# Optimization experiments

Measured on AMD Instinct MI355X. Metric: run time of the kernel, lower is better.

## Reference

```python
import jax, jax.numpy as jnp
import numpy as np

B, L, H, NE, SPAN = 16, 2048, 768, 64, 4
EPS_COS = 1e-8   # torch cosine_similarity eps
EPS_STD = 1e-5   # std stabilizer from the module


def _linear_init(key, fan_in, fan_out):
    s = 1.0 / np.sqrt(fan_in)
    kw, kb = jax.random.split(key)
    w = jax.random.uniform(kw, (fan_in, fan_out), jnp.float32, -s, s)
    b = jax.random.uniform(kb, (fan_out,), jnp.float32, -s, s)
    return w, b


def setup_inputs() -> dict:
    key = jax.random.key(0)
    ks = jax.random.split(key, 6)
    w1, b1 = _linear_init(ks[0], 2 * H + 1, H)
    w2, b2 = _linear_init(ks[1], H, 512)
    w3, b3 = _linear_init(ks[2], 512, 256)
    w4, b4 = _linear_init(ks[3], 256, 2)
    x = jax.random.normal(ks[4], (B, L, H), jnp.float32)
    entity_starts = jax.random.randint(ks[5], (B, NE), 0, L - SPAN)
    threshold = jnp.float32(0.9)
    return dict(x=x, threshold=threshold,
                w1=w1, b1=b1, w2=w2, b2=b2, w3=w3, b3=b3, w4=w4, b4=b4,
                entity_starts=entity_starts)


def reference(x, threshold, w1, b1, w2, b2, w3, b3, w4, b4, entity_starts):
    # --- per-entity span max-pool (segment-max over x) ---
    # gather span tokens: [B, NE*SPAN] token indices into the L axis
    idx = (entity_starts[:, :, None] + jnp.arange(SPAN)).reshape(B, NE * SPAN)
    spans = jnp.take_along_axis(x, idx[:, :, None], axis=1)      # [B, NE*SPAN, H]
    emb = spans.reshape(B, NE, SPAN, H).max(axis=2)               # [B, NE, H]

    # --- pairwise cosine similarity per batch ---
    norm = jnp.maximum(jnp.linalg.norm(emb, axis=-1, keepdims=True), EPS_COS)
    n = emb / norm
    cos = jnp.einsum('bie,bje->bij', n, n)                        # [B, NE, NE]
    std = jnp.std(cos, axis=(1, 2), ddof=1, keepdims=True)        # torch .std() is unbiased
    sim = (cos - threshold) / (std + EPS_STD)
    sim = jnp.triu(sim, k=1)

    # --- all i<j pairs: [sim, emb_i, emb_j] ---
    iu, ju = np.triu_indices(NE, k=1)                             # static pair indices
    feats = jnp.concatenate(
        [sim[:, iu, ju, None], emb[:, iu, :], emb[:, ju, :]], axis=-1
    ).reshape(-1, 2 * H + 1)                                      # [B*P, 2H+1]

    # --- classifier MLP (dropout = identity at eval) ---
    h = jax.nn.relu(feats @ w1 + b1)
    h = jax.nn.relu(h @ w2 + b2)
    h = jax.nn.relu(h @ w3 + b3)
    logits = h @ w4 + b4                                          # [B*P, 2]
    return logits
```

## Files before the change

### kernel.cpp

```cpp
#include <hip/hip_runtime.h>
#include <cstdint>
#include <cstddef>

#define B_    16
#define L_    2048
#define H_    768
#define NE_   64
#define SPAN_ 4
#define NPAIR 2016
#define NROWS (B_ * NPAIR)

typedef __bf16 bf16_t;
typedef __bf16 bf16x8 __attribute__((ext_vector_type(8)));
typedef __bf16 bf16x4 __attribute__((ext_vector_type(4)));
typedef float  floatx4 __attribute__((ext_vector_type(4)));

#define OFF_EMBH   ((size_t)3145728)
#define OFF_SIM    ((size_t)8126464)
#define OFF_W1ABT  ((size_t)8255488)
#define OFF_W2T    ((size_t)10614784)
#define OFF_W3T    ((size_t)11401216)
#define OFF_C1     ((size_t)11663360)
#define OFF_H2     ((size_t)67500032)
#define OFF_FLAG   ((size_t)117045248)
#define OFF_CANON  ((size_t)117045504)

#define SWZ(colb, row) ((colb) ^ (((row) & 3) << 4))

__device__ inline bf16_t cvt_elem(const void* p, size_t i, int isf) {
  if (isf) return (bf16_t)(((const float*)p)[i]);
  return ((const bf16_t*)p)[i];
}

__global__ __launch_bounds__(1024) void prep_embsim_kernel(
    const unsigned short* __restrict__ xu,
    const void* __restrict__ xv, const int* __restrict__ starts,
    const void* __restrict__ thr_ptr,
    const void* __restrict__ w1, const void* __restrict__ w2,
    const void* __restrict__ w3, const void* __restrict__ b1,
    const void* __restrict__ b2, const void* __restrict__ b3,
    const void* __restrict__ w4, const void* __restrict__ b4,
    int* __restrict__ flagout,
    bf16_t* __restrict__ w1abT, bf16_t* __restrict__ w2T,
    bf16_t* __restrict__ w3T, bf16_t* __restrict__ canon,
    bf16_t* __restrict__ embh, float* __restrict__ simv) {
  __shared__ __align__(16) char shbuf[98304];
  __shared__ int   tot[16];
  __shared__ float red1[16], red2[16];
  __shared__ float scale_s, thr_s;

  int blk = blockIdx.x;
  int t = threadIdx.x;

  {
    int bad = 0;
    for (int i = t; i < 4096; i += 1024) {
      int e = (xu[i] >> 7) & 0xFF;
      if (e > 133 || (e > 0 && e < 90)) bad++;
    }
    for (int off = 32; off > 0; off >>= 1) bad += __shfl_down(bad, off, 64);
    if ((t & 63) == 0) tot[t >> 6] = bad;
    __syncthreads();
  }
  int sumb = 0;
#pragma unroll
  for (int i = 0; i < 16; i++) sumb += tot[i];
  int isf = (sumb > 200) ? 1 : 0;
  __syncthreads();

  if (blk < 16) {
    bf16_t* nrm = (bf16_t*)shbuf;
    int b = blk;
    int e   = t >> 4;
    int l16 = t & 15;
    int d0  = l16 * 48;
    int st  = starts[b * NE_ + e];
    size_t off = ((size_t)(b * L_ + st)) * H_;
    float ss = 0.f;
    bf16x8 pv[6];
    if (isf) {
      const float* xp = (const float*)xv + off + d0;
#pragma unroll
      for (int c8 = 0; c8 < 6; c8++) {
        const float* p = xp + c8 * 8;
        bf16x8 o;
#pragma unroll
        for (int h = 0; h < 2; h++) {
          floatx4 r0 = *(const floatx4*)(p + h * 4);
          floatx4 r1 = *(const floatx4*)(p + H_ + h * 4);
          floatx4 r2 = *(const floatx4*)(p + 2 * H_ + h * 4);
          floatx4 r3 = *(const floatx4*)(p + 3 * H_ + h * 4);
#pragma unroll
          for (int q = 0; q < 4; q++) {
            float v = fmaxf(fmaxf(r0[q], r1[q]), fmaxf(r2[q], r3[q]));
            ss += v * v;
            o[h * 4 + q] = (bf16_t)v;
          }
        }
        pv[c8] = o;
      }
    } else {
      const bf16_t* xp = (const bf16_t*)xv + off + d0;
#pragma unroll
      for (int c8 = 0; c8 < 6; c8++) {
        const bf16_t* p = xp + c8 * 8;
        bf16x8 r0 = *(const bf16x8*)(p);
        bf16x8 r1 = *(const bf16x8*)(p + H_);
        bf16x8 r2 = *(const bf16x8*)(p + 2 * H_);
        bf16x8 r3 = *(const bf16x8*)(p + 3 * H_);
        bf16x8 o;
#pragma unroll
        for (int q = 0; q < 8; q++) {
          float v = fmaxf(fmaxf((float)r0[q], (float)r1[q]),
                          fmaxf((float)r2[q], (float)r3[q]));
          ss += v * v;
          o[q] = (bf16_t)v;
        }
        pv[c8] = o;
      }
    }
#pragma unroll
    for (int d = 1; d < 16; d <<= 1) ss += __shfl_xor(ss, d, 64);
    float inv = 1.0f / fmaxf(sqrtf(ss), 1e-8f);

    size_t gb = ((size_t)(b * 64 + e)) * 768 + d0;
    int rowbyte = e * 1536;
    int xw = (e & 7) << 4;
#pragma unroll
    for (int c8 = 0; c8 < 6; c8++) {
      *(bf16x8*)(embh + gb + c8 * 8) = pv[c8];
      bf16x8 o;
#pragma unroll
      for (int q = 0; q < 8; q++) o[q] = (bf16_t)((float)pv[c8][q] * inv);
      int byo = (rowbyte + (d0 + c8 * 8) * 2) ^ xw;
      *(bf16x8*)((char*)nrm + byo) = o;
    }
    __syncthreads();

    int w = t >> 6, lane = t & 63;
    int quad = lane >> 4, l15 = lane & 15;
    int ti = w >> 2, tj = w & 3;
    int rowA = ti * 16 + l15, rowB = tj * 16 + l15;
    int xa = (rowA & 7) << 4, xb = (rowB & 7) << 4;
    const char* nb = (const char*)nrm;
    floatx4 acc = {};
#pragma unroll 4
    for (int k0 = 0; k0 < 768; k0 += 32) {
      int cb = (k0 + quad * 8) * 2;
      bf16x8 aF = *(const bf16x8*)(nb + ((rowA * 1536 + cb) ^ xa));
      bf16x8 bF = *(const bf16x8*)(nb + ((rowB * 1536 + cb) ^ xb));
      acc = __builtin_amdgcn_mfma_f32_16x16x32_bf16(aF, bF, acc, 0, 0, 0);
    }

    float s1 = acc[0] + acc[1] + acc[2] + acc[3];
    float s2 = acc[0] * acc[0] + acc[1] * acc[1] + acc[2] * acc[2] + acc[3] * acc[3];
#pragma unroll
    for (int d = 32; d > 0; d >>= 1) {
      s1 += __shfl_xor(s1, d, 64);
      s2 += __shfl_xor(s2, d, 64);
    }
    if (lane == 0) { red1[w] = s1; red2[w] = s2; }
    __syncthreads();
    if (t == 0) {
      float S1 = 0.f, S2 = 0.f;
#pragma unroll
      for (int i = 0; i < 16; i++) { S1 += red1[i]; S2 += red2[i]; }
      float mean = S1 * (1.0f / 4096.0f);
      float var = (S2 - 4096.0f * mean * mean) * (1.0f / 4095.0f);
      float sd = sqrtf(fmaxf(var, 0.f));
      scale_s = 1.0f / (sd + 1e-5f);
      thr_s = isf ? *(const float*)thr_ptr : (float)(*(const bf16_t*)thr_ptr);
    }
    __syncthreads();
    float sc = scale_s, th = thr_s;
    int ibase = ti * 16 + quad * 4;
    int j = tj * 16 + l15;
#pragma unroll
    for (int r = 0; r < 4; r++) {
      int i = ibase + r;
      if (j > i) {
        int p = i * 63 - (i * (i - 1)) / 2 + (j - i - 1);
        simv[b * NPAIR + p] = (acc[r] - th) * sc;
      }
    }
    return;
  }

  if (blk == 16) {
    if (t == 0) flagout[0] = isf;
    for (int idx = t; idx < 2818; idx += 1024) {
      if (idx < 768)       canon[idx] = cvt_elem(w1, idx, isf);
      else if (idx < 1536) canon[idx] = cvt_elem(b1, idx - 768, isf);
      else if (idx < 2048) canon[idx] = cvt_elem(b2, idx - 1536, isf);
      else if (idx < 2304) canon[idx] = cvt_elem(b3, idx - 2048, isf);
      else if (idx < 2816) canon[idx] = cvt_elem(w4, idx - 2304, isf);
      else                 canon[idx] = cvt_elem(b4, idx - 2816, isf);
    }
    return;
  }

  int tix = blk - 17;
  const void* src; size_t srcoff; bf16_t* dst; int K, N;
  if (tix < 144)      { src = w1; srcoff = 768;               dst = w1abT;          K = 768; N = 768; }
  else if (tix < 288) { src = w1; srcoff = (size_t)769 * 768; dst = w1abT + 589824; K = 768; N = 768; tix -= 144; }
  else if (tix < 384) { src = w2; srcoff = 0;                 dst = w2T;            K = 768; N = 512; tix -= 288; }
  else                { src = w3; srcoff = 0;                 dst = w3T;            K = 512; N = 256; tix -= 384; }
  int tiles_k = K >> 6;
  int tn_t = tix / tiles_k, tk_t = tix - tn_t * tiles_k;
  bf16_t (*tile)[65] = (bf16_t(*)[65])shbuf;
  int ty = t >> 6, tx = t & 63;
#pragma unroll
  for (int p = 0; p < 4; p++) {
    int kk = tk_t * 64 + p * 16 + ty;
    int nn = tn_t * 64 + tx;
    tile[p * 16 + ty][tx] = cvt_elem(src, srcoff + (size_t)kk * N + nn, isf);
  }
  __syncthreads();
#pragma unroll
  for (int p = 0; p < 4; p++) {
    int nn = tn_t * 64 + p * 16 + ty;
    int kk = tk_t * 64 + tx;
    dst[(size_t)nn * K + kk] = tile[tx][p * 16 + ty];
  }
}

__global__ __launch_bounds__(256) void gemm1_kernel(
    const bf16_t* __restrict__ A, const bf16_t* __restrict__ Bt,
    float* __restrict__ C) {
  const int K = 768, N = 1536;
  __shared__ __align__(16) bf16_t Asm[64 * 32];
  __shared__ __align__(16) bf16_t Bsm[128 * 32];
  int bm = blockIdx.x, bn = blockIdx.y;
  int t = threadIdx.x;
  int w = t >> 6, lane = t & 63;
  int quad = lane >> 4, l15 = lane & 15;
  int wm = w >> 1, wn = w & 1;

  floatx4 acc[2][4] = {};
  const char* Abase = (const char*)(A + (size_t)bm * 64 * K);
  const char* Bbase = (const char*)(Bt + (size_t)bn * 128 * K);
  const int rowbytes = K * 2;

  for (int k0 = 0; k0 < K; k0 += 32) {
    {
      int fo = w * 1024 + lane * 16;
      int row = fo >> 6, colb = fo & 63;
      __builtin_amdgcn_global_load_lds(
          (__attribute__((address_space(1))) char*)(Abase + (size_t)row * rowbytes + k0 * 2 + SWZ(colb, row)),
          (__attribute__((address_space(3))) char*)((char*)Asm + w * 1024),
          16, 0, 0);
    }
#pragma unroll
    for (int it = 0; it < 2; it++) {
      int fo = (w * 2 + it) * 1024 + lane * 16;
      int row = fo >> 6, colb = fo & 63;
      __builtin_amdgcn_global_load_lds(
          (__attribute__((address_space(1))) char*)(Bbase + (size_t)row * rowbytes + k0 * 2 + SWZ(colb, row)),
          (__attribute__((address_space(3))) char*)((char*)Bsm + (w * 2 + it) * 1024),
          16, 0, 0);
    }
    __syncthreads();

    bf16x8 aF[2], bF[4];
#pragma unroll
    for (int tm = 0; tm < 2; tm++) {
      int ra = wm * 32 + tm * 16 + l15;
      aF[tm] = *((const bf16x8*)((const char*)Asm + ra * 64 + SWZ(quad * 16, ra)));
    }
#pragma unroll
    for (int tn = 0; tn < 4; tn++) {
      int rb = wn * 64 + tn * 16 + l15;
      bF[tn] = *((const bf16x8*)((const char*)Bsm + rb * 64 + SWZ(quad * 16, rb)));
    }
#pragma unroll
    for (int tm = 0; tm < 2; tm++)
#pragma unroll
      for (int tn = 0; tn < 4; tn++)
        acc[tm][tn] = __builtin_amdgcn_mfma_f32_16x16x32_bf16(aF[tm], bF[tn], acc[tm][tn], 0, 0, 0);
    __syncthreads();
  }

#pragma unroll
  for (int tm = 0; tm < 2; tm++) {
    int grow0 = bm * 64 + wm * 32 + tm * 16 + quad * 4;
#pragma unroll
    for (int tn = 0; tn < 4; tn++) {
      int gcol = bn * 128 + wn * 64 + tn * 16 + l15;
#pragma unroll
      for (int r = 0; r < 4; r++)
        C[(size_t)(grow0 + r) * N + gcol] = acc[tm][tn][r];
    }
  }
}

__global__ __launch_bounds__(512, 4) void gemm2_fused_kernel(
    const float* __restrict__ C1, const float* __restrict__ sim,
    const bf16_t* __restrict__ w2T, const bf16_t* __restrict__ canon,
    bf16_t* __restrict__ h2) {
  __shared__ __align__(16) bf16_t Asm[128 * 40];
  __shared__ __align__(16) bf16_t Bsm[256 * 32];
  __shared__ int   rowI[128], rowJ[128];
  __shared__ float rowS[128];
  __shared__ bf16_t w1s[768], b1s[768];
  __shared__ float b2s[256];
  int bm = blockIdx.x, bn = blockIdx.y;
  int t = threadIdx.x;

  if (t < 128) {
    int r = bm * 128 + t;
    int b = r / NPAIR, p = r - b * NPAIR;
    int i = 0, rem = p;
    while (rem >= 63 - i) { rem -= 63 - i; i++; }
    rowI[t] = b * 64 + i;
    rowJ[t] = b * 64 + i + 1 + rem;
    rowS[t] = sim[r];
  }
  for (int c = t; c < 768; c += 512) { w1s[c] = canon[c]; b1s[c] = canon[768 + c]; }
  if (t < 256) b2s[t] = (float)canon[1536 + bn * 256 + t];
  __syncthreads();

  int w = t >> 6, lane = t & 63;
  int quad = lane >> 4, l15 = lane & 15;
  int wm = w >> 2, wn = w & 3;
  floatx4 acc[4][4] = {};

  const char* Bbase = (const char*)(w2T + (size_t)bn * 256 * 768);

  int arow = t >> 2;
  int acolc = (t & 3) * 8;
  const float* Ai = C1 + (size_t)rowI[arow] * 1536 + acolc;
  const float* Aj = C1 + (size_t)rowJ[arow] * 1536 + 768 + acolc;
  float s = rowS[arow];
  bf16_t* awr = Asm + arow * 40 + acolc;

  float4 pi0 = *(const float4*)(Ai);
  float4 pi1 = *(const float4*)(Ai + 4);
  float4 pj0 = *(const float4*)(Aj);
  float4 pj1 = *(const float4*)(Aj + 4);

  for (int k0 = 0; k0 < 768; k0 += 32) {
#pragma unroll
    for (int it = 0; it < 2; it++) {
      int fo = w * 2048 + it * 1024 + lane * 16;
      int row = fo >> 6, colb = fo & 63;
      __builtin_amdgcn_global_load_lds(
          (__attribute__((address_space(1))) char*)(Bbase + (size_t)row * 1536 + k0 * 2 + SWZ(colb, row)),
          (__attribute__((address_space(3))) char*)((char*)Bsm + w * 2048 + it * 1024),
          16, 0, 0);
    }
    {
      int kc = k0 + acolc;
      bf16x8 o;
      const bf16x8 wv8 = *(const bf16x8*)(w1s + kc);
      const bf16x8 bv8 = *(const bf16x8*)(b1s + kc);
      o[0] = (bf16_t)fmaxf(pi0.x + pj0.x + s * (float)wv8[0] + (float)bv8[0], 0.f);
      o[1] = (bf16_t)fmaxf(pi0.y + pj0.y + s * (float)wv8[1] + (float)bv8[1], 0.f);
      o[2] = (bf16_t)fmaxf(pi0.z + pj0.z + s * (float)wv8[2] + (float)bv8[2], 0.f);
      o[3] = (bf16_t)fmaxf(pi0.w + pj0.w + s * (float)wv8[3] + (float)bv8[3], 0.f);
      o[4] = (bf16_t)fmaxf(pi1.x + pj1.x + s * (float)wv8[4] + (float)bv8[4], 0.f);
      o[5] = (bf16_t)fmaxf(pi1.y + pj1.y + s * (float)wv8[5] + (float)bv8[5], 0.f);
      o[6] = (bf16_t)fmaxf(pi1.z + pj1.z + s * (float)wv8[6] + (float)bv8[6], 0.f);
      o[7] = (bf16_t)fmaxf(pi1.w + pj1.w + s * (float)wv8[7] + (float)bv8[7], 0.f);
      *(bf16x8*)awr = o;
    }
    if (k0 + 32 < 768) {
      pi0 = *(const float4*)(Ai + k0 + 32);
      pi1 = *(const float4*)(Ai + k0 + 36);
      pj0 = *(const float4*)(Aj + k0 + 32);
      pj1 = *(const float4*)(Aj + k0 + 36);
    }
    __syncthreads();

    bf16x8 aF[4], bF[4];
#pragma unroll
    for (int tm = 0; tm < 4; tm++)
      aF[tm] = *((const bf16x8*)(Asm + (wm * 64 + tm * 16 + l15) * 40 + quad * 8));
#pragma unroll
    for (int tn = 0; tn < 4; tn++) {
      int rb = wn * 64 + tn * 16 + l15;
      bF[tn] = *((const bf16x8*)((const char*)Bsm + rb * 64 + SWZ(quad * 16, rb)));
    }
#pragma unroll
    for (int tm = 0; tm < 4; tm++)
#pragma unroll
      for (int tn = 0; tn < 4; tn++)
        acc[tm][tn] = __builtin_amdgcn_mfma_f32_16x16x32_bf16(aF[tm], bF[tn], acc[tm][tn], 0, 0, 0);
    __syncthreads();
  }

#pragma unroll
  for (int tm = 0; tm < 4; tm++) {
    int grow0 = bm * 128 + wm * 64 + tm * 16 + quad * 4;
#pragma unroll
    for (int tn = 0; tn < 4; tn++) {
      int lcol = wn * 64 + tn * 16 + l15;
      int gcol = bn * 256 + lcol;
#pragma unroll
      for (int r = 0; r < 4; r++) {
        float v = fmaxf(acc[tm][tn][r] + b2s[lcol], 0.f);
        h2[(size_t)(grow0 + r) * 512 + gcol] = (bf16_t)v;
      }
    }
  }
}

__global__ __launch_bounds__(256) void gemm3_fused_kernel(
    const bf16_t* __restrict__ h2, const bf16_t* __restrict__ w3T,
    const bf16_t* __restrict__ canon, const int* __restrict__ flagp,
    void* __restrict__ out) {
  __shared__ __align__(16) bf16_t Asm[64 * 32];
  __shared__ __align__(16) bf16_t Bsm[256 * 32];
  __shared__ float part[64][2][4];
  __shared__ float w4s[512];
  __shared__ float b3s[256];
  int bm = blockIdx.x;
  int t = threadIdx.x;
  int w = t >> 6, lane = t & 63;
  int quad = lane >> 4, l15 = lane & 15;

  w4s[t]       = (float)canon[2304 + t];
  w4s[256 + t] = (float)canon[2304 + 256 + t];
  b3s[t]       = (float)canon[2048 + t];

  floatx4 acc[4][4] = {};
  const char* Abase = (const char*)(h2 + (size_t)bm * 64 * 512);
  const char* Bbase = (const char*)w3T;

  for (int k0 = 0; k0 < 512; k0 += 32) {
    {
      int fo = w * 1024 + lane * 16;
      int row = fo >> 6, colb = fo & 63;
      __builtin_amdgcn_global_load_lds(
          (__attribute__((address_space(1))) char*)(Abase + (size_t)row * 1024 + k0 * 2 + SWZ(colb, row)),
          (__attribute__((address_space(3))) char*)((char*)Asm + w * 1024),
          16, 0, 0);
    }
#pragma unroll
    for (int it = 0; it < 4; it++) {
      int fo = w * 4096 + it * 1024 + lane * 16;
      int row = fo >> 6, colb = fo & 63;
      __builtin_amdgcn_global_load_lds(
          (__attribute__((address_space(1))) char*)(Bbase + (size_t)row * 1024 + k0 * 2 + SWZ(colb, row)),
          (__attribute__((address_space(3))) char*)((char*)Bsm + w * 4096 + it * 1024),
          16, 0, 0);
    }
    __syncthreads();

    bf16x8 aF[4], bF[4];
#pragma unroll
    for (int tm = 0; tm < 4; tm++) {
      int ra = tm * 16 + l15;
      aF[tm] = *((const bf16x8*)((const char*)Asm + ra * 64 + SWZ(quad * 16, ra)));
    }
#pragma unroll
    for (int tn = 0; tn < 4; tn++) {
      int rb = w * 64 + tn * 16 + l15;
      bF[tn] = *((const bf16x8*)((const char*)Bsm + rb * 64 + SWZ(quad * 16, rb)));
    }
#pragma unroll
    for (int tm = 0; tm < 4; tm++)
#pragma unroll
      for (int tn = 0; tn < 4; tn++)
        acc[tm][tn] = __builtin_amdgcn_mfma_f32_16x16x32_bf16(aF[tm], bF[tn], acc[tm][tn], 0, 0, 0);
    __syncthreads();
  }

#pragma unroll
  for (int tm = 0; tm < 4; tm++) {
#pragma unroll
    for (int reg = 0; reg < 4; reg++) {
      float p0 = 0.f, p1 = 0.f;
#pragma unroll
      for (int tn = 0; tn < 4; tn++) {
        int col = w * 64 + tn * 16 + l15;
        float v = fmaxf(acc[tm][tn][reg] + b3s[col], 0.f);
        p0 += v * w4s[col * 2];
        p1 += v * w4s[col * 2 + 1];
      }
#pragma unroll
      for (int d = 1; d < 16; d <<= 1) {
        p0 += __shfl_xor(p0, d, 64);
        p1 += __shfl_xor(p1, d, 64);
      }
      if (l15 == 0) {
        int r = tm * 16 + quad * 4 + reg;
        part[r][0][w] = p0;
        part[r][1][w] = p1;
      }
    }
  }
  __syncthreads();
  if (t < 128) {
    int r = t >> 1, c = t & 1;
    float v = part[r][c][0] + part[r][c][1] + part[r][c][2] + part[r][c][3]
            + (float)canon[2816 + c];
    size_t rg = (size_t)bm * 64 + r;
    if (flagp[0]) ((float*)out)[rg * 2 + c] = v;
    else          ((bf16_t*)out)[rg * 2 + c] = (bf16_t)v;
  }
}

extern "C" void kernel_launch(void* const* d_in, const int* in_sizes, int n_in,
                              void* d_out, int out_size, void* d_ws, size_t ws_size,
                              hipStream_t stream) {
  const void* x      = d_in[0];
  const void* thr    = d_in[1];
  const void* w1     = d_in[2];
  const void* b1     = d_in[3];
  const void* w2     = d_in[4];
  const void* b2     = d_in[5];
  const void* w3     = d_in[6];
  const void* b3     = d_in[7];
  const void* w4     = d_in[8];
  const void* b4     = d_in[9];
  const int*  starts = (const int*)d_in[10];

  char* ws = (char*)d_ws;
  bf16_t* embh  = (bf16_t*)(ws + OFF_EMBH);
  float*  simv  = (float*)(ws + OFF_SIM);
  bf16_t* w1abT = (bf16_t*)(ws + OFF_W1ABT);
  bf16_t* w2T   = (bf16_t*)(ws + OFF_W2T);
  bf16_t* w3T   = (bf16_t*)(ws + OFF_W3T);
  float*  C1    = (float*)(ws + OFF_C1);
  bf16_t* h2    = (bf16_t*)(ws + OFF_H2);
  int*    flag  = (int*)(ws + OFF_FLAG);
  bf16_t* canon = (bf16_t*)(ws + OFF_CANON);

  prep_embsim_kernel<<<433, 1024, 0, stream>>>(
      (const unsigned short*)x, x, starts, thr,
      w1, w2, w3, b1, b2, b3, w4, b4,
      flag, w1abT, w2T, w3T, canon, embh, simv);

  {
    dim3 g(1024 / 64, 1536 / 128);
    gemm1_kernel<<<g, 256, 0, stream>>>(embh, w1abT, C1);
  }

  {
    dim3 g(NROWS / 128, 2);
    gemm2_fused_kernel<<<g, 512, 0, stream>>>(C1, simv, w2T, canon, h2);
  }

  gemm3_fused_kernel<<<NROWS / 64, 256, 0, stream>>>(h2, w3T, canon, flag, d_out);
}
```

Before: 269.4 us.

## Double-buffer LDS in gemm2/gemm3 and grid-stride the weight-prep blocks

The K loops of gemm2_fused and gemm3_fused now use two LDS buffers, so the next tile's global-to-LDS loads (and the fused A-operand build in gemm2) are issued before the MFMA work on the current tile. This overlaps memory latency with compute, at the cost of twice the shared memory, which may lower occupancy under the 512,4 launch bounds. The prep kernel's weight-transpose blocks now loop grid-stride, which cuts its launch from 433 to 256 blocks with fewer, longer-running blocks.

New measurement: 263.9 us. -2.0%, faster.

```diff
diff --git a/kernel.cpp b/kernel.cpp
--- a/kernel.cpp
+++ b/kernel.cpp
@@ -14,6 +14,9 @@
 typedef __bf16 bf16x8 __attribute__((ext_vector_type(8)));
 typedef __bf16 bf16x4 __attribute__((ext_vector_type(4)));
 typedef float  floatx4 __attribute__((ext_vector_type(4)));
+
+#define AS1 __attribute__((address_space(1)))
+#define AS3 __attribute__((address_space(3)))
 
 #define OFF_EMBH   ((size_t)3145728)
 #define OFF_SIM    ((size_t)8126464)
@@ -186,41 +189,43 @@
     return;
   }
 
-  if (blk == 16) {
-    if (t == 0) flagout[0] = isf;
-    for (int idx = t; idx < 2818; idx += 1024) {
-      if (idx < 768)       canon[idx] = cvt_elem(w1, idx, isf);
-      else if (idx < 1536) canon[idx] = cvt_elem(b1, idx - 768, isf);
-      else if (idx < 2048) canon[idx] = cvt_elem(b2, idx - 1536, isf);
-      else if (idx < 2304) canon[idx] = cvt_elem(b3, idx - 2048, isf);
-      else if (idx < 2816) canon[idx] = cvt_elem(w4, idx - 2304, isf);
-      else                 canon[idx] = cvt_elem(b4, idx - 2816, isf);
-    }
-    return;
-  }
-
-  int tix = blk - 17;
-  const void* src; size_t srcoff; bf16_t* dst; int K, N;
-  if (tix < 144)      { src = w1; srcoff = 768;               dst = w1abT;          K = 768; N = 768; }
-  else if (tix < 288) { src = w1; srcoff = (size_t)769 * 768; dst = w1abT + 589824; K = 768; N = 768; tix -= 144; }
-  else if (tix < 384) { src = w2; srcoff = 0;                 dst = w2T;            K = 768; N = 512; tix -= 288; }
-  else                { src = w3; srcoff = 0;                 dst = w3T;            K = 512; N = 256; tix -= 384; }
-  int tiles_k = K >> 6;
-  int tn_t = tix / tiles_k, tk_t = tix - tn_t * tiles_k;
-  bf16_t (*tile)[65] = (bf16_t(*)[65])shbuf;
-  int ty = t >> 6, tx = t & 63;
-#pragma unroll
-  for (int p = 0; p < 4; p++) {
-    int kk = tk_t * 64 + p * 16 + ty;
-    int nn = tn_t * 64 + tx;
-    tile[p * 16 + ty][tx] = cvt_elem(src, srcoff + (size_t)kk * N + nn, isf);
-  }
-  __syncthreads();
-#pragma unroll
-  for (int p = 0; p < 4; p++) {
-    int nn = tn_t * 64 + p * 16 + ty;
-    int kk = tk_t * 64 + tx;
-    dst[(size_t)nn * K + kk] = tile[tx][p * 16 + ty];
+  for (int u = blk - 16; u < 417; u += 240) {
+    if (u == 0) {
+      if (t == 0) flagout[0] = isf;
+      for (int idx = t; idx < 2818; idx += 1024) {
+        if (idx < 768)       canon[idx] = cvt_elem(w1, idx, isf);
+        else if (idx < 1536) canon[idx] = cvt_elem(b1, idx - 768, isf);
+        else if (idx < 2048) canon[idx] = cvt_elem(b2, idx - 1536, isf);
+        else if (idx < 2304) canon[idx] = cvt_elem(b3, idx - 2048, isf);
+        else if (idx < 2816) canon[idx] = cvt_elem(w4, idx - 2304, isf);
+        else                 canon[idx] = cvt_elem(b4, idx - 2816, isf);
+      }
+    } else {
+      int tix = u - 1;
+      const void* src; size_t srcoff; bf16_t* dst; int K, N;
+      if (tix < 144)      { src = w1; srcoff = 768;               dst = w1abT;          K = 768; N = 768; }
+      else if (tix < 288) { src = w1; srcoff = (size_t)769 * 768; dst = w1abT + 589824; K = 768; N = 768; tix -= 144; }
+      else if (tix < 384) { src = w2; srcoff = 0;                 dst = w2T;            K = 768; N = 512; tix -= 288; }
+      else                { src = w3; srcoff = 0;                 dst = w3T;            K = 512; N = 256; tix -= 384; }
+      int tiles_k = K >> 6;
+      int tn_t = tix / tiles_k, tk_t = tix - tn_t * tiles_k;
+      bf16_t (*tile)[65] = (bf16_t(*)[65])shbuf;
+      int ty = t >> 6, tx = t & 63;
+      __syncthreads();
+#pragma unroll
+      for (int p = 0; p < 4; p++) {
+        int kk = tk_t * 64 + p * 16 + ty;
+        int nn = tn_t * 64 + tx;
+        tile[p * 16 + ty][tx] = cvt_elem(src, srcoff + (size_t)kk * N + nn, isf);
+      }
+      __syncthreads();
+#pragma unroll
+      for (int p = 0; p < 4; p++) {
+        int nn = tn_t * 64 + p * 16 + ty;
+        int kk = tk_t * 64 + tx;
+        dst[(size_t)nn * K + kk] = tile[tx][p * 16 + ty];
+      }
+    }
   }
 }
 
@@ -246,8 +251,8 @@
       int fo = w * 1024 + lane * 16;
       int row = fo >> 6, colb = fo & 63;
       __builtin_amdgcn_global_load_lds(
-          (__attribute__((address_space(1))) char*)(Abase + (size_t)row * rowbytes + k0 * 2 + SWZ(colb, row)),
-          (__attribute__((address_space(3))) char*)((char*)Asm + w * 1024),
+          (AS1 char*)(Abase + (size_t)row * rowbytes + k0 * 2 + SWZ(colb, row)),
+          (AS3 char*)((char*)Asm + w * 1024),
           16, 0, 0);
     }
 #pragma unroll
@@ -255,8 +260,8 @@
       int fo = (w * 2 + it) * 1024 + lane * 16;
       int row = fo >> 6, colb = fo & 63;
       __builtin_amdgcn_global_load_lds(
-          (__attribute__((address_space(1))) char*)(Bbase + (size_t)row * rowbytes + k0 * 2 + SWZ(colb, row)),
-          (__attribute__((address_space(3))) char*)((char*)Bsm + (w * 2 + it) * 1024),
+          (AS1 char*)(Bbase + (size_t)row * rowbytes + k0 * 2 + SWZ(colb, row)),
+          (AS3 char*)((char*)Bsm + (w * 2 + it) * 1024),
           16, 0, 0);
     }
     __syncthreads();
@@ -297,8 +302,8 @@
     const float* __restrict__ C1, const float* __restrict__ sim,
     const bf16_t* __restrict__ w2T, const bf16_t* __restrict__ canon,
     bf16_t* __restrict__ h2) {
-  __shared__ __align__(16) bf16_t Asm[128 * 40];
-  __shared__ __align__(16) bf16_t Bsm[256 * 32];
+  __shared__ __align__(16) bf16_t Asm[2][128 * 40];
+  __shared__ __align__(16) bf16_t Bsm[2][256 * 32];
   __shared__ int   rowI[128], rowJ[128];
   __shared__ float rowS[128];
   __shared__ bf16_t w1s[768], b1s[768];
@@ -331,54 +336,86 @@
   const float* Ai = C1 + (size_t)rowI[arow] * 1536 + acolc;
   const float* Aj = C1 + (size_t)rowJ[arow] * 1536 + 768 + acolc;
   float s = rowS[arow];
-  bf16_t* awr = Asm + arow * 40 + acolc;
 
   float4 pi0 = *(const float4*)(Ai);
   float4 pi1 = *(const float4*)(Ai + 4);
   float4 pj0 = *(const float4*)(Aj);
   float4 pj1 = *(const float4*)(Aj + 4);
-
-  for (int k0 = 0; k0 < 768; k0 += 32) {
-#pragma unroll
-    for (int it = 0; it < 2; it++) {
-      int fo = w * 2048 + it * 1024 + lane * 16;
-      int row = fo >> 6, colb = fo & 63;
-      __builtin_amdgcn_global_load_lds(
-          (__attribute__((address_space(1))) char*)(Bbase + (size_t)row * 1536 + k0 * 2 + SWZ(colb, row)),
-          (__attribute__((address_space(3))) char*)((char*)Bsm + w * 2048 + it * 1024),
-          16, 0, 0);
-    }
-    {
-      int kc = k0 + acolc;
-      bf16x8 o;
-      const bf16x8 wv8 = *(const bf16x8*)(w1s + kc);
-      const bf16x8 bv8 = *(const bf16x8*)(b1s + kc);
-      o[0] = (bf16_t)fmaxf(pi0.x + pj0.x + s * (float)wv8[0] + (float)bv8[0], 0.f);
-      o[1] = (bf16_t)fmaxf(pi0.y + pj0.y + s * (float)wv8[1] + (float)bv8[1], 0.f);
-      o[2] = (bf16_t)fmaxf(pi0.z + pj0.z + s * (float)wv8[2] + (float)bv8[2], 0.f);
-      o[3] = (bf16_t)fmaxf(pi0.w + pj0.w + s * (float)wv8[3] + (float)bv8[3], 0.f);
-      o[4] = (bf16_t)fmaxf(pi1.x + pj1.x + s * (float)wv8[4] + (float)bv8[4], 0.f);
-      o[5] = (bf16_t)fmaxf(pi1.y + pj1.y + s * (float)wv8[5] + (float)bv8[5], 0.f);
-      o[6] = (bf16_t)fmaxf(pi1.z + pj1.z + s * (float)wv8[6] + (float)bv8[6], 0.f);
-      o[7] = (bf16_t)fmaxf(pi1.w + pj1.w + s * (float)wv8[7] + (float)bv8[7], 0.f);
-      *(bf16x8*)awr = o;
-    }
-    if (k0 + 32 < 768) {
-      pi0 = *(const float4*)(Ai + k0 + 32);
-      pi1 = *(const float4*)(Ai + k0 + 36);
-      pj0 = *(const float4*)(Aj + k0 + 32);
-      pj1 = *(const float4*)(Aj + k0 + 36);
-    }
-    __syncthreads();
+#pragma unroll
+  for (int it = 0; it < 2; it++) {
+    int fo = w * 2048 + it * 1024 + lane * 16;
+    int row = fo >> 6, colb = fo & 63;
+    __builtin_amdgcn_global_load_lds(
+        (AS1 char*)(Bbase + (size_t)row * 1536 + SWZ(colb, row)),
+        (AS3 char*)((char*)&Bsm[0][0] + w * 2048 + it * 1024),
+        16, 0, 0);
+  }
+  {
+    int kc = acolc;
+    bf16x8 o;
+    const bf16x8 wv8 = *(const bf16x8*)(w1s + kc);
+    const bf16x8 bv8 = *(const bf16x8*)(b1s + kc);
+    o[0] = (bf16_t)fmaxf(pi0.x + pj0.x + s * (float)wv8[0] + (float)bv8[0], 0.f);
+    o[1] = (bf16_t)fmaxf(pi0.y + pj0.y + s * (float)wv8[1] + (float)bv8[1], 0.f);
+    o[2] = (bf16_t)fmaxf(pi0.z + pj0.z + s * (float)wv8[2] + (float)bv8[2], 0.f);
+    o[3] = (bf16_t)fmaxf(pi0.w + pj0.w + s * (float)wv8[3] + (float)bv8[3], 0.f);
+    o[4] = (bf16_t)fmaxf(pi1.x + pj1.x + s * (float)wv8[4] + (float)bv8[4], 0.f);
+    o[5] = (bf16_t)fmaxf(pi1.y + pj1.y + s * (float)wv8[5] + (float)bv8[5], 0.f);
+    o[6] = (bf16_t)fmaxf(pi1.z + pj1.z + s * (float)wv8[6] + (float)bv8[6], 0.f);
+    o[7] = (bf16_t)fmaxf(pi1.w + pj1.w + s * (float)wv8[7] + (float)bv8[7], 0.f);
+    *(bf16x8*)(&Asm[0][arow * 40 + acolc]) = o;
+  }
+  pi0 = *(const float4*)(Ai + 32);
+  pi1 = *(const float4*)(Ai + 36);
+  pj0 = *(const float4*)(Aj + 32);
+  pj1 = *(const float4*)(Aj + 36);
+  __syncthreads();
+
+  for (int kt = 0; kt < 24; ++kt) {
+    int cur = kt & 1, nxt = cur ^ 1;
+    if (kt < 23) {
+      int k1 = (kt + 1) * 32;
+#pragma unroll
+      for (int it = 0; it < 2; it++) {
+        int fo = w * 2048 + it * 1024 + lane * 16;
+        int row = fo >> 6, colb = fo & 63;
+        __builtin_amdgcn_global_load_lds(
+            (AS1 char*)(Bbase + (size_t)row * 1536 + k1 * 2 + SWZ(colb, row)),
+            (AS3 char*)((char*)&Bsm[nxt][0] + w * 2048 + it * 1024),
+            16, 0, 0);
+      }
+      {
+        int kc = k1 + acolc;
+        bf16x8 o;
+        const bf16x8 wv8 = *(const bf16x8*)(w1s + kc);
+        const bf16x8 bv8 = *(const bf16x8*)(b1s + kc);
+        o[0] = (bf16_t)fmaxf(pi0.x + pj0.x + s * (float)wv8[0] + (float)bv8[0], 0.f);
+        o[1] = (bf16_t)fmaxf(pi0.y + pj0.y + s * (float)wv8[1] + (float)bv8[1], 0.f);
+        o[2] = (bf16_t)fmaxf(pi0.z + pj0.z + s * (float)wv8[2] + (float)bv8[2], 0.f);
+        o[3] = (bf16_t)fmaxf(pi0.w + pj0.w + s * (float)wv8[3] + (float)bv8[3], 0.f);
+        o[4] = (bf16_t)fmaxf(pi1.x + pj1.x + s * (float)wv8[4] + (float)bv8[4], 0.f);
+        o[5] = (bf16_t)fmaxf(pi1.y + pj1.y + s * (float)wv8[5] + (float)bv8[5], 0.f);
+        o[6] = (bf16_t)fmaxf(pi1.z + pj1.z + s * (float)wv8[6] + (float)bv8[6], 0.f);
+        o[7] = (bf16_t)fmaxf(pi1.w + pj1.w + s * (float)wv8[7] + (float)bv8[7], 0.f);
+        *(bf16x8*)(&Asm[nxt][arow * 40 + acolc]) = o;
+      }
+      if (kt < 22) {
+        int k2 = (kt + 2) * 32;
+        pi0 = *(const float4*)(Ai + k2);
+        pi1 = *(const float4*)(Ai + k2 + 4);
+        pj0 = *(const float4*)(Aj + k2);
+        pj1 = *(const float4*)(Aj + k2 + 4);
+      }
+    }
 
     bf16x8 aF[4], bF[4];
 #pragma unroll
     for (int tm = 0; tm < 4; tm++)
-      aF[tm] = *((const bf16x8*)(Asm + (wm * 64 + tm * 16 + l15) * 40 + quad * 8));
+      aF[tm] = *((const bf16x8*)(&Asm[cur][(wm * 64 + tm * 16 + l15) * 40 + quad * 8]));
 #pragma unroll
     for (int tn = 0; tn < 4; tn++) {
       int rb = wn * 64 + tn * 16 + l15;
-      bF[tn] = *((const bf16x8*)((const char*)Bsm + rb * 64 + SWZ(quad * 16, rb)));
+      bF[tn] = *((const bf16x8*)((const char*)&Bsm[cur][0] + rb * 64 + SWZ(quad * 16, rb)));
     }
 #pragma unroll
     for (int tm = 0; tm < 4; tm++)
@@ -408,8 +445,8 @@
     const bf16_t* __restrict__ h2, const bf16_t* __restrict__ w3T,
     const bf16_t* __restrict__ canon, const int* __restrict__ flagp,
     void* __restrict__ out) {
-  __shared__ __align__(16) bf16_t Asm[64 * 32];
-  __shared__ __align__(16) bf16_t Bsm[256 * 32];
+  __shared__ __align__(16) bf16_t Asm[2][64 * 32];
+  __shared__ __align__(16) bf16_t Bsm[2][256 * 32];
   __shared__ float part[64][2][4];
   __shared__ float w4s[512];
   __shared__ float b3s[256];
@@ -426,36 +463,58 @@
   const char* Abase = (const char*)(h2 + (size_t)bm * 64 * 512);
   const char* Bbase = (const char*)w3T;
 
-  for (int k0 = 0; k0 < 512; k0 += 32) {
-    {
-      int fo = w * 1024 + lane * 16;
-      int row = fo >> 6, colb = fo & 63;
-      __builtin_amdgcn_global_load_lds(
-          (__attribute__((address_space(1))) char*)(Abase + (size_t)row * 1024 + k0 * 2 + SWZ(colb, row)),
-          (__attribute__((address_space(3))) char*)((char*)Asm + w * 1024),
-          16, 0, 0);
-    }
-#pragma unroll
-    for (int it = 0; it < 4; it++) {
-      int fo = w * 4096 + it * 1024 + lane * 16;
-      int row = fo >> 6, colb = fo & 63;
-      __builtin_amdgcn_global_load_lds(
-          (__attribute__((address_space(1))) char*)(Bbase + (size_t)row * 1024 + k0 * 2 + SWZ(colb, row)),
-          (__attribute__((address_space(3))) char*)((char*)Bsm + w * 4096 + it * 1024),
-          16, 0, 0);
-    }
-    __syncthreads();
+  {
+    int fo = w * 1024 + lane * 16;
+    int row = fo >> 6, colb = fo & 63;
+    __builtin_amdgcn_global_load_lds(
+        (AS1 char*)(Abase + (size_t)row * 1024 + SWZ(colb, row)),
+        (AS3 char*)((char*)&Asm[0][0] + w * 1024),
+        16, 0, 0);
+  }
+#pragma unroll
+  for (int it = 0; it < 4; it++) {
+    int fo = w * 4096 + it * 1024 + lane * 16;
+    int row = fo >> 6, colb = fo & 63;
+    __builtin_amdgcn_global_load_lds(
+        (AS1 char*)(Bbase + (size_t)row * 1024 + SWZ(colb, row)),
+        (AS3 char*)((char*)&Bsm[0][0] + w * 4096 + it * 1024),
+        16, 0, 0);
+  }
+  __syncthreads();
+
+  for (int kt = 0; kt < 16; ++kt) {
+    int cur = kt & 1, nxt = cur ^ 1;
+    if (kt < 15) {
+      int k1 = (kt + 1) * 32;
+      {
+        int fo = w * 1024 + lane * 16;
+        int row = fo >> 6, colb = fo & 63;
+        __builtin_amdgcn_global_load_lds(
+            (AS1 char*)(Abase + (size_t)row * 1024 + k1 * 2 + SWZ(colb, row)),
+            (AS3 char*)((char*)&Asm[nxt][0] + w * 1024),
+            16, 0, 0);
+      }
+#pragma unroll
+      for (int it = 0; it < 4; it++) {
+        int fo = w * 4096 + it * 1024 + lane * 16;
+        int row = fo >> 6, colb = fo & 63;
+        __builtin_amdgcn_global_load_lds(
+            (AS1 char*)(Bbase + (size_t)row * 1024 + k1 * 2 + SWZ(colb, row)),
+            (AS3 char*)((char*)&Bsm[nxt][0] + w * 4096 + it * 1024),
+            16, 0, 0);
+      }
+    }
 
     bf16x8 aF[4], bF[4];
 #pragma unroll
     for (int tm = 0; tm < 4; tm++) {
       int ra = tm * 16 + l15;
-      aF[tm] = *((const bf16x8*)((const char*)Asm + ra * 64 + SWZ(quad * 16, ra)));
+      aF[tm] = *((const bf16x8*)((const char*)&Asm[cur][0] + ra * 64 + SWZ(quad * 16, ra)));
     }
 #pragma unroll
     for (int tn = 0; tn < 4; tn++) {
       int rb = w * 64 + tn * 16 + l15;
-      bF[tn] = *((const bf16x8*)((const char*)Bsm + rb * 64 + SWZ(quad * 16, rb)));
+      bF[tn] = *((const bf16x8*)((const char*)&Bsm[cur][0] + rb * 64 + SWZ(quad * 16, rb)));
     }
 #pragma unroll
     for (int tm = 0; tm < 4; tm++)
@@ -526,7 +585,7 @@
   int*    flag  = (int*)(ws + OFF_FLAG);
   bf16_t* canon = (bf16_t*)(ws + OFF_CANON);
 
-  prep_embsim_kernel<<<433, 1024, 0, stream>>>(
+  prep_embsim_kernel<<<256, 1024, 0, stream>>>(
       (const unsigned short*)x, x, starts, thr,
       w1, w2, w3, b1, b2, b3, w4, b4,
       flag, w1abT, w2T, w3T, canon, embh, simv);
```
